# Performance work log

Measured on AMD Instinct MI355X. Metric: run time of the kernel, lower is better.

Reference implementation:

```python
import jax, jax.numpy as jnp
import numpy as np

D_MODEL = 2048
N_HEAD = 16
N_KV_HEAD = 4
D_HEAD = D_MODEL // N_HEAD          # 128
N_REP = N_HEAD // N_KV_HEAD        # 4
B, S = 2, 2048


def setup_inputs() -> dict:
    key = jax.random.key(0)
    ks = jax.random.split(key, 7)
    x = jax.random.normal(ks[0], (B, S, D_MODEL), dtype=jnp.float32)
    cos = jax.random.uniform(ks[1], (S, D_HEAD // 2), dtype=jnp.float32)
    sin = jax.random.uniform(ks[2], (S, D_HEAD // 2), dtype=jnp.float32)
    sc = 1.0 / np.sqrt(D_MODEL)
    # weights stored as [in, out] so projection is x @ W
    wq = jax.random.normal(ks[3], (D_MODEL, D_MODEL), dtype=jnp.float32) * sc
    wk = jax.random.normal(ks[4], (D_MODEL, N_KV_HEAD * D_HEAD), dtype=jnp.float32) * sc
    wv = jax.random.normal(ks[5], (D_MODEL, N_KV_HEAD * D_HEAD), dtype=jnp.float32) * sc
    wo = jax.random.normal(ks[6], (D_MODEL, D_MODEL), dtype=jnp.float32) * sc
    return {"x": x, "cos": cos, "sin": sin, "wq": wq, "wk": wk, "wv": wv, "wo": wo}


def _apply_rope(t, cos, sin):
    # t: [B, H, S, D_HEAD]; cos/sin: [S, D_HEAD//2]
    d = t.shape[-1] // 2
    t1, t2 = t[..., :d], t[..., d:]
    c = cos[None, None, :, :]
    s = sin[None, None, :, :]
    return jnp.concatenate([t1 * c - t2 * s, t2 * c + t1 * s], axis=-1)


def reference(x, cos, sin, wq, wk, wv, wo):
    b, s, _ = x.shape
    q = (x @ wq).reshape(b, s, N_HEAD, D_HEAD).transpose(0, 2, 1, 3)      # [B,H,S,d]
    k = (x @ wk).reshape(b, s, N_KV_HEAD, D_HEAD).transpose(0, 2, 1, 3)   # [B,Hk,S,d]
    v = (x @ wv).reshape(b, s, N_KV_HEAD, D_HEAD).transpose(0, 2, 1, 3)
    q = _apply_rope(q, cos, sin)
    k = _apply_rope(k, cos, sin)
    # group query heads by shared kv head (repeat_interleave => consecutive groups)
    qg = q.reshape(b, N_KV_HEAD, N_REP, s, D_HEAD)
    scale = 1.0 / jnp.sqrt(jnp.asarray(D_HEAD, dtype=q.dtype))
    scores = jnp.einsum('bkrsd,bktd->bkrst', qg, k) * scale               # [B,Hk,r,S,S]
    causal = jnp.tril(jnp.ones((s, s), dtype=bool))
    scores = jnp.where(causal, scores, jnp.asarray(-jnp.inf, dtype=scores.dtype))
    attn = jax.nn.softmax(scores, axis=-1)
    out = jnp.einsum('bkrst,bktd->bkrsd', attn, v)                        # [B,Hk,r,S,d]
    out = out.reshape(b, N_HEAD, s, D_HEAD).transpose(0, 2, 1, 3).reshape(b, s, D_MODEL)
    return out @ wo
```

## Files before the change

kernel.cpp:

```cpp
#include <hip/hip_runtime.h>
#include <stdint.h>

#define D_MODEL 2048
#define NHEAD 16
#define NKV 4
#define DHEAD 128
#define BB 2
#define SS 2048
#define MROWS (BB*SS)
#define NQKV 3072

typedef __bf16 bf16x8_t __attribute__((ext_vector_type(8)));
typedef float f32x4_t __attribute__((ext_vector_type(4)));
typedef float f32x16_t __attribute__((ext_vector_type(16)));
typedef unsigned short u16x8_t __attribute__((ext_vector_type(8)));
typedef unsigned short u16x4_t __attribute__((ext_vector_type(4)));
typedef unsigned int u32x4_t __attribute__((ext_vector_type(4)));

__device__ __forceinline__ unsigned short f2bf(float f) {
    return __builtin_bit_cast(unsigned short, (__bf16)f);
}
__device__ __forceinline__ float bf2f(unsigned short h) {
    union { uint32_t u; float f; } v; v.u = ((uint32_t)h) << 16;
    return v.f;
}
__device__ __forceinline__ unsigned int pack_bf2(float lo, float hi) {
    return (unsigned int)f2bf(lo) | ((unsigned int)f2bf(hi) << 16);
}

__device__ __forceinline__ void stage16(const unsigned short* g, unsigned short* l) {
    auto gp = (const __attribute__((address_space(1))) unsigned short*)(uintptr_t)g;
    auto lp = (__attribute__((address_space(3))) unsigned short*)(uint32_t)(uintptr_t)l;
    __builtin_amdgcn_global_load_lds(gp, lp, 16, 0, 0);
}
__device__ __forceinline__ bf16x8_t lds_frag(const unsigned short* p) {
    return __builtin_bit_cast(bf16x8_t, *(const u16x8_t*)p);
}

#define BAR()   do { __builtin_amdgcn_s_barrier(); asm volatile("" ::: "memory"); } while (0)
#define WAITL() asm volatile("s_waitcnt lgkmcnt(0)" ::: "memory")

__global__ void k_convert(const float* __restrict__ in, unsigned short* __restrict__ out, int n4) {
    int stride = gridDim.x * blockDim.x;
    for (int idx = blockIdx.x * blockDim.x + threadIdx.x; idx < n4; idx += stride) {
        float4 f = ((const float4*)in)[idx];
        u16x4_t o;
        o[0] = f2bf(f.x); o[1] = f2bf(f.y); o[2] = f2bf(f.z); o[3] = f2bf(f.w);
        ((u16x4_t*)out)[idx] = o;
    }
}

__global__ __launch_bounds__(256) void k_transpose(const float* __restrict__ in,
                                                   unsigned short* __restrict__ out,
                                                   int R, int C) {
    __shared__ unsigned short tile[64][72];
    const int c0 = blockIdx.x * 64, r0 = blockIdx.y * 64;
    const int t = threadIdx.x;
    #pragma unroll
    for (int i = 0; i < 4; i++) {
        int g = i * 256 + t;
        int r = g >> 4, c4 = (g & 15) * 4;
        float4 f = *(const float4*)&in[(size_t)(r0 + r) * C + c0 + c4];
        tile[r][c4 + 0] = f2bf(f.x); tile[r][c4 + 1] = f2bf(f.y);
        tile[r][c4 + 2] = f2bf(f.z); tile[r][c4 + 3] = f2bf(f.w);
    }
    __syncthreads();
    #pragma unroll
    for (int i = 0; i < 2; i++) {
        int g = i * 256 + t;
        int oc = g >> 3, r8 = (g & 7) * 8;
        u16x8_t o;
        #pragma unroll
        for (int k = 0; k < 8; k++) o[k] = tile[r8 + k][oc];
        *(u16x8_t*)&out[(size_t)(c0 + oc) * R + r0 + r8] = o;
    }
}

__global__ void k_rope(const unsigned short* __restrict__ in, const float* __restrict__ cosb,
                       const float* __restrict__ sinb, unsigned short* __restrict__ out,
                       int nheads, int in_row_stride, float scale) {
    int idx = blockIdx.x * blockDim.x + threadIdx.x;
    int total = BB * SS * nheads * 64;
    if (idx >= total) return;
    int d  = idx & 63;
    int hh = (idx >> 6) % nheads;
    int bs = (idx >> 6) / nheads;
    int s  = bs % SS, b = bs / SS;
    const unsigned short* ip = in + (size_t)(b * SS + s) * in_row_stride + hh * 128 + d;
    float t1 = bf2f(ip[0]), t2 = bf2f(ip[64]);
    float c = cosb[s * 64 + d], sn = sinb[s * 64 + d];
    unsigned short* op = out + ((size_t)(b * nheads + hh) * SS + s) * 128 + d;
    op[0]  = f2bf((t1 * c - t2 * sn) * scale);
    op[64] = f2bf((t2 * c + t1 * sn) * scale);
}

__global__ __launch_bounds__(256) void k_vtrans(const unsigned short* __restrict__ src,
                                                unsigned short* __restrict__ vt,
                                                int stride, int colbase) {
    const int s0 = blockIdx.x * 64;
    const int kvb = blockIdx.y;
    const int b = kvb >> 2, kv = kvb & 3;
    __shared__ unsigned short tile[64][136];
    const int t = threadIdx.x;
    #pragma unroll
    for (int i = 0; i < 4; i++) {
        int g = i * 256 + t;
        int sr = g >> 4, c8 = (g & 15) * 8;
        u16x8_t v = *(const u16x8_t*)&src[(size_t)(b * SS + s0 + sr) * stride + colbase + kv * 128 + c8];
        #pragma unroll
        for (int k = 0; k < 8; k++) tile[sr][c8 + k] = v[k];
    }
    __syncthreads();
    unsigned short* obase = vt + (size_t)kvb * DHEAD * SS;
    #pragma unroll
    for (int i = 0; i < 4; i++) {
        int g = i * 256 + t;
        int d = g >> 3, s8 = (g & 7) * 8;
        u16x8_t o;
        #pragma unroll
        for (int k = 0; k < 8; k++) o[k] = tile[s8 + k][d];
        *(u16x8_t*)&obase[(size_t)d * SS + s0 + s8] = o;
    }
}

template <bool OUTF32>
__global__ __launch_bounds__(512, 2) void k_gemm8(const unsigned short* __restrict__ A,
                                                  const unsigned short* __restrict__ Bt,
                                                  void* __restrict__ Cout,
                                                  int N, int K, int ntn) {
    __shared__ __align__(16) unsigned short As[2][256 * 64];
    __shared__ __align__(16) unsigned short Bs[2][256 * 64];
    const int nwg = gridDim.x, wg = blockIdx.x;
    const int qq = nwg >> 3, rr = nwg & 7;
    const int xcd = wg & 7, sid = wg >> 3;
    const int swg = (xcd < rr ? xcd * (qq + 1) : rr * (qq + 1) + (xcd - rr) * qq) + sid;
    const int m0 = (swg / ntn) * 256, n0 = (swg % ntn) * 256;

    const int tid = threadIdx.x, lane = tid & 63, wid = tid >> 6;
    const int lr = lane & 15, lg = lane >> 4;
    const int wr = (wid >> 2) * 128, wc = (wid & 3) * 64;
    const int NT = K >> 6;

    auto stage = [&](int tile, int pos) {
        int srcTile = tile < NT ? tile : NT - 1;
        bool isA = (pos == 0) || (pos == 3);
        int half = (pos >= 2) ? 1 : 0;
        const unsigned short* base = isA ? A : Bt;
        int row0 = (isA ? m0 : n0) + half * 128;
        unsigned short* lbase = (isA ? As[tile & 1] : Bs[tile & 1]) + half * 8192;
        int k0 = srcTile * 64;
        #pragma unroll
        for (int i = 0; i < 2; i++) {
            int g = i * 512 + tid;
            int row = g >> 3, p = g & 7;
            stage16(&base[(size_t)(row0 + row) * K + k0 + ((p ^ (row & 7)) * 8)],
                    &lbase[(i * 512 + wid * 64) * 8]);
        }
    };

    bf16x8_t aA[4][2], bLo[2][2], bHi[2][2];
    f32x4_t acc[8][4] = {};

    stage(0, 0); stage(0, 3); stage(0, 1); stage(0, 2);
    stage(1, 1); stage(1, 2);
    asm volatile("s_waitcnt vmcnt(4)" ::: "memory");
    BAR();

    for (int t = 0; t < NT; t++) {
        const unsigned short* as = As[t & 1];
        const unsigned short* bs = Bs[t & 1];
        #pragma unroll
        for (int i = 0; i < 4; i++)
          #pragma unroll
          for (int kk = 0; kk < 2; kk++) {
            int R = wr + i * 16 + lr;
            aA[i][kk] = lds_frag(&as[R * 64 + (((kk * 4 + lg) ^ (R & 7)) * 8)]);
          }
        #pragma unroll
        for (int j = 0; j < 2; j++)
          #pragma unroll
          for (int kk = 0; kk < 2; kk++) {
            int R = wc + j * 16 + lr;
            bLo[j][kk] = lds_frag(&bs[R * 64 + (((kk * 4 + lg) ^ (R & 7)) * 8)]);
          }
        stage(t + 1, 0);
        BAR(); WAITL();
        __builtin_amdgcn_s_setprio(1);
        #pragma unroll
        for (int kk = 0; kk < 2; kk++)
          #pragma unroll
          for (int i = 0; i < 4; i++)
            #pragma unroll
            for (int j = 0; j < 2; j++)
              acc[i][j] = __builtin_amdgcn_mfma_f32_16x16x32_bf16(aA[i][kk], bLo[j][kk], acc[i][j], 0, 0, 0);
        __builtin_amdgcn_s_setprio(0);
        BAR();
        #pragma unroll
        for (int j = 0; j < 2; j++)
          #pragma unroll
          for (int kk = 0; kk < 2; kk++) {
            int R = wc + (2 + j) * 16 + lr;
            bHi[j][kk] = lds_frag(&bs[R * 64 + (((kk * 4 + lg) ^ (R & 7)) * 8)]);
          }
        stage(t + 1, 3);
        BAR(); WAITL();
        __builtin_amdgcn_s_setprio(1);
        #pragma unroll
        for (int kk = 0; kk < 2; kk++)
          #pragma unroll
          for (int i = 0; i < 4; i++)
            #pragma unroll
            for (int j = 0; j < 2; j++)
              acc[i][2 + j] = __builtin_amdgcn_mfma_f32_16x16x32_bf16(aA[i][kk], bHi[j][kk], acc[i][2 + j], 0, 0, 0);
        __builtin_amdgcn_s_setprio(0);
        BAR();
        #pragma unroll
        for (int i = 0; i < 4; i++)
          #pragma unroll
          for (int kk = 0; kk < 2; kk++) {
            int R = wr + (4 + i) * 16 + lr;
            aA[i][kk] = lds_frag(&as[R * 64 + (((kk * 4 + lg) ^ (R & 7)) * 8)]);
          }
        stage(t + 2, 1);
        BAR(); WAITL();
        __builtin_amdgcn_s_setprio(1);
        #pragma unroll
        for (int kk = 0; kk < 2; kk++)
          #pragma unroll
          for (int i = 0; i < 4; i++)
            #pragma unroll
            for (int j = 0; j < 2; j++)
              acc[4 + i][2 + j] = __builtin_amdgcn_mfma_f32_16x16x32_bf16(aA[i][kk], bHi[j][kk], acc[4 + i][2 + j], 0, 0, 0);
        __builtin_amdgcn_s_setprio(0);
        BAR();
        stage(t + 2, 2);
        asm volatile("s_waitcnt vmcnt(4)" ::: "memory");
        BAR(); WAITL();
        __builtin_amdgcn_s_setprio(1);
        #pragma unroll
        for (int kk = 0; kk < 2; kk++)
          #pragma unroll
          for (int i = 0; i < 4; i++)
            #pragma unroll
            for (int j = 0; j < 2; j++)
              acc[4 + i][j] = __builtin_amdgcn_mfma_f32_16x16x32_bf16(aA[i][kk], bLo[j][kk], acc[4 + i][j], 0, 0, 0);
        __builtin_amdgcn_s_setprio(0);
        BAR();
    }

    #pragma unroll
    for (int m = 0; m < 8; m++)
      #pragma unroll
      for (int n = 0; n < 4; n++)
        #pragma unroll
        for (int r = 0; r < 4; r++) {
            int row = m0 + wr + m * 16 + lg * 4 + r;
            int col = n0 + wc + n * 16 + lr;
            if constexpr (OUTF32) ((float*)Cout)[(size_t)row * N + col] = acc[m][n][r];
            else ((unsigned short*)Cout)[(size_t)row * N + col] = f2bf(acc[m][n][r]);
        }
}

template <bool OUTF32>
__global__ __launch_bounds__(512, 2) void k_gemm8h(const unsigned short* __restrict__ A,
                                                   const unsigned short* __restrict__ Bt,
                                                   void* __restrict__ Cout,
                                                   int N, int K, int ntn) {
    __shared__ __align__(16) unsigned short As[2][128 * 64];
    __shared__ __align__(16) unsigned short Bs[2][256 * 64];
    const int nwg = gridDim.x, wg = blockIdx.x;
    const int qq = nwg >> 3, rr = nwg & 7;
    const int xcd = wg & 7, sid = wg >> 3;
    const int swg = (xcd < rr ? xcd * (qq + 1) : rr * (qq + 1) + (xcd - rr) * qq) + sid;
    const int m0 = (swg / ntn) * 128, n0 = (swg % ntn) * 256;

    const int tid = threadIdx.x, lane = tid & 63, wid = tid >> 6;
    const int lr = lane & 15, lg = lane >> 4;
    const int wr = (wid >> 2) * 64, wc = (wid & 3) * 64;
    const int NT = K >> 6;

    auto stage = [&](int tile, int pos) {
        int srcTile = tile < NT ? tile : NT - 1;
        bool isA = (pos == 0);
        const unsigned short* base = isA ? A : Bt;
        int row0 = isA ? m0 : (n0 + (pos - 1) * 128);
        unsigned short* lbase = isA ? As[tile & 1] : (Bs[tile & 1] + (pos - 1) * 8192);
        int k0 = srcTile * 64;
        #pragma unroll
        for (int i = 0; i < 2; i++) {
            int g = i * 512 + tid;
            int row = g >> 3, p = g & 7;
            stage16(&base[(size_t)(row0 + row) * K + k0 + ((p ^ (row & 7)) * 8)],
                    &lbase[(i * 512 + wid * 64) * 8]);
        }
    };

    bf16x8_t aA[2][2], bLo[2][2], bHi[2][2];
    f32x4_t acc[4][4] = {};

    stage(0, 0); stage(0, 1); stage(0, 2);
    stage(1, 1); stage(1, 2);
    asm volatile("s_waitcnt vmcnt(4)" ::: "memory");
    BAR();

    for (int t = 0; t < NT; t++) {
        const unsigned short* as = As[t & 1];
        const unsigned short* bs = Bs[t & 1];
        #pragma unroll
        for (int i = 0; i < 2; i++)
          #pragma unroll
          for (int kk = 0; kk < 2; kk++) {
            int R = wr + i * 16 + lr;
            aA[i][kk] = lds_frag(&as[R * 64 + (((kk * 4 + lg) ^ (R & 7)) * 8)]);
          }
        #pragma unroll
        for (int j = 0; j < 2; j++)
          #pragma unroll
          for (int kk = 0; kk < 2; kk++) {
            int R = wc + j * 16 + lr;
            bLo[j][kk] = lds_frag(&bs[R * 64 + (((kk * 4 + lg) ^ (R & 7)) * 8)]);
          }
        stage(t + 1, 0);
        BAR(); WAITL();
        __builtin_amdgcn_s_setprio(1);
        #pragma unroll
        for (int kk = 0; kk < 2; kk++)
          #pragma unroll
          for (int i = 0; i < 2; i++)
            #pragma unroll
            for (int j = 0; j < 2; j++)
              acc[i][j] = __builtin_amdgcn_mfma_f32_16x16x32_bf16(aA[i][kk], bLo[j][kk], acc[i][j], 0, 0, 0);
        __builtin_amdgcn_s_setprio(0);
        BAR();
        #pragma unroll
        for (int j = 0; j < 2; j++)
          #pragma unroll
          for (int kk = 0; kk < 2; kk++) {
            int R = wc + (2 + j) * 16 + lr;
            bHi[j][kk] = lds_frag(&bs[R * 64 + (((kk * 4 + lg) ^ (R & 7)) * 8)]);
          }
        BAR(); WAITL();
        __builtin_amdgcn_s_setprio(1);
        #pragma unroll
        for (int kk = 0; kk < 2; kk++)
          #pragma unroll
          for (int i = 0; i < 2; i++)
            #pragma unroll
            for (int j = 0; j < 2; j++)
              acc[i][2 + j] = __builtin_amdgcn_mfma_f32_16x16x32_bf16(aA[i][kk], bHi[j][kk], acc[i][2 + j], 0, 0, 0);
        __builtin_amdgcn_s_setprio(0);
        BAR();
        #pragma unroll
        for (int i = 0; i < 2; i++)
          #pragma unroll
          for (int kk = 0; kk < 2; kk++) {
            int R = wr + (2 + i) * 16 + lr;
            aA[i][kk] = lds_frag(&as[R * 64 + (((kk * 4 + lg) ^ (R & 7)) * 8)]);
          }
        stage(t + 2, 1);
        BAR(); WAITL();
        __builtin_amdgcn_s_setprio(1);
        #pragma unroll
        for (int kk = 0; kk < 2; kk++)
          #pragma unroll
          for (int i = 0; i < 2; i++)
            #pragma unroll
            for (int j = 0; j < 2; j++)
              acc[2 + i][2 + j] = __builtin_amdgcn_mfma_f32_16x16x32_bf16(aA[i][kk], bHi[j][kk], acc[2 + i][2 + j], 0, 0, 0);
        __builtin_amdgcn_s_setprio(0);
        BAR();
        stage(t + 2, 2);
        asm volatile("s_waitcnt vmcnt(4)" ::: "memory");
        BAR(); WAITL();
        __builtin_amdgcn_s_setprio(1);
        #pragma unroll
        for (int kk = 0; kk < 2; kk++)
          #pragma unroll
          for (int i = 0; i < 2; i++)
            #pragma unroll
            for (int j = 0; j < 2; j++)
              acc[2 + i][j] = __builtin_amdgcn_mfma_f32_16x16x32_bf16(aA[i][kk], bLo[j][kk], acc[2 + i][j], 0, 0, 0);
        __builtin_amdgcn_s_setprio(0);
        BAR();
    }

    #pragma unroll
    for (int m = 0; m < 4; m++)
      #pragma unroll
      for (int n = 0; n < 4; n++)
        #pragma unroll
        for (int r = 0; r < 4; r++) {
            int row = m0 + wr + m * 16 + lg * 4 + r;
            int col = n0 + wc + n * 16 + lr;
            if constexpr (OUTF32) ((float*)Cout)[(size_t)row * N + col] = acc[m][n][r];
            else ((unsigned short*)Cout)[(size_t)row * N + col] = f2bf(acc[m][n][r]);
        }
}

__global__ __launch_bounds__(256, 2) void k_attn(const unsigned short* __restrict__ qg,
                                                 const float* __restrict__ cosb,
                                                 const float* __restrict__ sinb,
                                                 const unsigned short* __restrict__ kb,
                                                 const unsigned short* __restrict__ vt,
                                                 unsigned short* __restrict__ ab) {
    const int bid = blockIdx.x;
    const int u = bid & 255;
    const int t = (bid < 256) ? (u >> 5) : (15 - (u >> 5));
    const int h = u & 15, b = (u >> 4) & 1;
    const int kvh = h >> 2;
    const int tid = threadIdx.x, lane = tid & 63, wid = tid >> 6;
    const int ql = lane & 31, hi = lane >> 5;
    const int swzq = ql & 7;
    __shared__ __align__(16) unsigned short k_lds[2][64 * 128];
    __shared__ __align__(16) unsigned short v_lds[2][128 * 64];
    __shared__ float sm_lds[128];

    const unsigned short* kbase = kb + (size_t)(b * NKV + kvh) * SS * DHEAD;
    const unsigned short* vbase = vt + (size_t)(b * NKV + kvh) * DHEAD * SS;

    auto stage_kv = [&](int j, int buf) {
        #pragma unroll
        for (int i = 0; i < 4; i++) {
            int g = i * 256 + wid * 64 + lane;
            int row = g >> 4, p = g & 15;
            stage16(&kbase[(size_t)(j * 64 + row) * DHEAD + ((p ^ (row & 7)) * 8)],
                    &k_lds[buf][(i * 256 + wid * 64) * 8]);
        }
        #pragma unroll
        for (int i = 0; i < 4; i++) {
            int g = i * 256 + wid * 64 + lane;
            int row = g >> 3, p = g & 7;
            stage16(&vbase[(size_t)row * SS + j * 64 + ((p ^ (row & 7)) * 8)],
                    &v_lds[buf][(i * 256 + wid * 64) * 8]);
        }
    };

    auto make_frag = [&](const f32x16_t& p, int base) -> bf16x8_t {
        unsigned int c01 = pack_bf2(p[base + 0], p[base + 1]);
        unsigned int c23 = pack_bf2(p[base + 2], p[base + 3]);
        unsigned int c45 = pack_bf2(p[base + 4], p[base + 5]);
        unsigned int c67 = pack_bf2(p[base + 6], p[base + 7]);
        unsigned int r1 = __shfl_xor(hi ? c01 : c45, 32);
        unsigned int r2 = __shfl_xor(hi ? c23 : c67, 32);
        u32x4_t w;
        w[0] = hi ? r1 : c01;
        w[1] = hi ? r2 : c23;
        w[2] = hi ? c45 : r1;
        w[3] = hi ? c67 : r2;
        return __builtin_bit_cast(bf16x8_t, w);
    };

    const int q0w = t * 128 + wid * 32;
    const int s_row = q0w + ql;
    const int jend = 2 * t + 1;

    bf16x8_t qf[8];
    {
        const unsigned short* qsrc = qg + (size_t)(b * SS + s_row) * NQKV + h * DHEAD;
        const float SCALE = 0.12751743f;
        #pragma unroll
        for (int kk = 0; kk < 4; kk++) {
            int dbase = kk * 16 + hi * 8;
            u16x8_t r1 = *(const u16x8_t*)&qsrc[dbase];
            u16x8_t r2 = *(const u16x8_t*)&qsrc[64 + dbase];
            float4 c0 = *(const float4*)&cosb[(size_t)s_row * 64 + dbase];
            float4 c1 = *(const float4*)&cosb[(size_t)s_row * 64 + dbase + 4];
            float4 s0 = *(const float4*)&sinb[(size_t)s_row * 64 + dbase];
            float4 s1 = *(const float4*)&sinb[(size_t)s_row * 64 + dbase + 4];
            float cc[8] = {c0.x, c0.y, c0.z, c0.w, c1.x, c1.y, c1.z, c1.w};
            float ss[8] = {s0.x, s0.y, s0.z, s0.w, s1.x, s1.y, s1.z, s1.w};
            #pragma unroll
            for (int e = 0; e < 8; e++) {
                float t1 = bf2f(r1[e]), t2 = bf2f(r2[e]);
                qf[kk][e]     = (__bf16)((t1 * cc[e] - t2 * ss[e]) * SCALE);
                qf[kk + 4][e] = (__bf16)((t2 * cc[e] + t1 * ss[e]) * SCALE);
            }
        }
    }

    f32x16_t acc[4] = {};
    float m_i = -1e30f, l_i = 0.f;

    stage_kv(0, 0);
    asm volatile("s_waitcnt vmcnt(0)" ::: "memory");
    __syncthreads();

    #pragma unroll 1
    for (int j = 0; j <= jend; j++) {
        const int buf = j & 1;
        if (j < jend) stage_kv(j + 1, buf ^ 1);
        if ((q0w + 31) >= (j << 6)) {
            const unsigned short* kl = k_lds[buf];
            const unsigned short* vl = v_lds[buf];
            f32x16_t p0 = {}, p1 = {};
            __builtin_amdgcn_s_setprio(1);
            #pragma unroll
            for (int kk = 0; kk < 8; kk++) {
                int c = ((2 * kk + hi) ^ swzq) * 8;
                bf16x8_t k0 = lds_frag(&kl[ql * 128 + c]);
                bf16x8_t k1 = lds_frag(&kl[(32 + ql) * 128 + c]);
                p0 = __builtin_amdgcn_mfma_f32_32x32x16_bf16(k0, qf[kk], p0, 0, 0, 0);
                p1 = __builtin_amdgcn_mfma_f32_32x32x16_bf16(k1, qf[kk], p1, 0, 0, 0);
            }
            __builtin_amdgcn_s_setprio(0);
            if ((j << 6) + 63 > q0w) {
                const int qg2 = q0w + ql;
                const int kvb = (j << 6) + 4 * hi;
                #pragma unroll
                for (int r = 0; r < 16; r++) {
                    int kvg = kvb + (r & 3) + 8 * (r >> 2);
                    if (kvg > qg2) p0[r] = -1e30f;
                    if (kvg + 32 > qg2) p1[r] = -1e30f;
                }
            }
            float mx = p0[0];
            #pragma unroll
            for (int r = 1; r < 16; r++) mx = fmaxf(mx, p0[r]);
            #pragma unroll
            for (int r = 0; r < 16; r++) mx = fmaxf(mx, p1[r]);
            mx = fmaxf(mx, __shfl_xor(mx, 32));
            if (__any(mx - m_i > 8.0f)) {
                float mnew = fmaxf(m_i, mx);
                float alpha = exp2f(m_i - mnew);
                l_i *= alpha; m_i = mnew;
                if (lane < 32) sm_lds[wid * 32 + lane] = alpha;
                WAITL();
                #pragma unroll
                for (int r = 0; r < 16; r++) {
                    float ar = sm_lds[wid * 32 + (r & 3) + 8 * (r >> 2) + 4 * hi];
                    #pragma unroll
                    for (int d = 0; d < 4; d++) acc[d][r] *= ar;
                }
            }
            float sum = 0.f;
            #pragma unroll
            for (int r = 0; r < 16; r++) { float v = exp2f(p0[r] - m_i); p0[r] = v; sum += v; }
            #pragma unroll
            for (int r = 0; r < 16; r++) { float v = exp2f(p1[r] - m_i); p1[r] = v; sum += v; }
            sum += __shfl_xor(sum, 32);
            l_i += sum;
            bf16x8_t pa[4];
            pa[0] = make_frag(p0, 0);
            pa[1] = make_frag(p0, 8);
            pa[2] = make_frag(p1, 0);
            pa[3] = make_frag(p1, 8);
            __builtin_amdgcn_s_setprio(1);
            #pragma unroll
            for (int ks = 0; ks < 4; ks++) {
                int cv = ((2 * ks + hi) ^ swzq) * 8;
                #pragma unroll
                for (int d = 0; d < 4; d++) {
                    bf16x8_t bv = lds_frag(&vl[(d * 32 + ql) * 64 + cv]);
                    acc[d] = __builtin_amdgcn_mfma_f32_32x32x16_bf16(pa[ks], bv, acc[d], 0, 0, 0);
                }
            }
            __builtin_amdgcn_s_setprio(0);
        }
        asm volatile("s_waitcnt vmcnt(0)" ::: "memory");
        __syncthreads();
    }

    if (lane < 32) sm_lds[wid * 32 + lane] = l_i;
    WAITL();
    #pragma unroll
    for (int r = 0; r < 16; r++) {
        float li = sm_lds[wid * 32 + (r & 3) + 8 * (r >> 2) + 4 * hi];
        float rl = 1.0f / li;
        int rowg = q0w + (r & 3) + 8 * (r >> 2) + 4 * hi;
        #pragma unroll
        for (int d = 0; d < 4; d++)
            ab[((size_t)b * SS + rowg) * D_MODEL + h * DHEAD + d * 32 + ql] =
                f2bf(acc[d][r] * rl);
    }
}

extern "C" void kernel_launch(void* const* d_in, const int* in_sizes, int n_in,
                              void* d_out, int out_size, void* d_ws, size_t ws_size,
                              hipStream_t stream) {
    const float* x    = (const float*)d_in[0];
    const float* cosb = (const float*)d_in[1];
    const float* sinb = (const float*)d_in[2];
    const float* wq   = (const float*)d_in[3];
    const float* wk   = (const float*)d_in[4];
    const float* wv   = (const float*)d_in[5];
    const float* wo   = (const float*)d_in[6];

    char* ws = (char*)d_ws;
    unsigned short* xb    = (unsigned short*)(ws + (size_t)0);
    unsigned short* wqkvT = (unsigned short*)(ws + ((size_t)16 << 20));
    unsigned short* woT   = (unsigned short*)(ws + ((size_t)28 << 20));
    unsigned short* qkvg  = (unsigned short*)(ws + ((size_t)36 << 20));
    unsigned short* abuf  = (unsigned short*)(ws + ((size_t)60 << 20));
    unsigned short* kbuf  = (unsigned short*)(ws + ((size_t)76 << 20));
    unsigned short* vtb   = (unsigned short*)(ws + ((size_t)80 << 20));

    k_convert<<<2048, 256, 0, stream>>>(x, xb, MROWS * D_MODEL / 4);
    k_transpose<<<dim3(32, 32), 256, 0, stream>>>(wq, wqkvT, D_MODEL, D_MODEL);
    k_transpose<<<dim3(8, 32), 256, 0, stream>>>(wk, wqkvT + (size_t)2048 * D_MODEL, D_MODEL, 512);
    k_transpose<<<dim3(8, 32), 256, 0, stream>>>(wv, wqkvT + (size_t)2560 * D_MODEL, D_MODEL, 512);
    k_transpose<<<dim3(32, 32), 256, 0, stream>>>(wo, woT, D_MODEL, D_MODEL);

    k_gemm8<false><<<16 * 12, 512, 0, stream>>>(xb, wqkvT, qkvg, NQKV, D_MODEL, 12);

    k_rope<<<(BB * SS * NKV * 64) / 256, 256, 0, stream>>>(qkvg + 2048, cosb, sinb, kbuf, NKV, NQKV, 1.0f);
    k_vtrans<<<dim3(32, 8), 256, 0, stream>>>(qkvg, vtb, NQKV, 2560);

    k_attn<<<512, 256, 0, stream>>>(qkvg, cosb, sinb, kbuf, vtb, abuf);

    k_gemm8h<true><<<32 * 8, 512, 0, stream>>>(abuf, woT, (float*)d_out, D_MODEL, D_MODEL, 8);
}
```

Measured before the change: 203.6 us.

## Merge weight transposes into one launch and remap attention blocks per XCD

Four separate weight-transpose launches become a single kernel that picks its source matrix from the block index, which saves launch overhead and gaps between kernels. The attention grid mapping is also reordered so that block ids sharing bid&7 (one XCD under round-robin dispatch) handle the same batch and KV head. This should keep each head's K/V tiles resident in that XCD's L2. Causal load balance is kept by pairing forward and reversed query tiles across the two halves of the grid.

```diff
diff --git a/kernel.cpp b/kernel.cpp
--- a/kernel.cpp
+++ b/kernel.cpp
@@ -50,11 +50,20 @@
     }
 }
 
-__global__ __launch_bounds__(256) void k_transpose(const float* __restrict__ in,
-                                                   unsigned short* __restrict__ out,
-                                                   int R, int C) {
+__global__ __launch_bounds__(256) void k_transpose_all(const float* __restrict__ wq,
+                                                       const float* __restrict__ wk,
+                                                       const float* __restrict__ wv,
+                                                       const float* __restrict__ wo,
+                                                       unsigned short* __restrict__ wqkvT,
+                                                       unsigned short* __restrict__ woT) {
+    int id = blockIdx.x;
+    const float* in; unsigned short* out; int R, C, cx, ry;
+    if (id < 1024)      { in = wq; out = wqkvT;                              R = 2048; C = 2048; cx = id & 31; ry = id >> 5; }
+    else if (id < 1280) { id -= 1024; in = wk; out = wqkvT + (size_t)2048 * 2048; R = 2048; C = 512; cx = id & 7; ry = id >> 3; }
+    else if (id < 1536) { id -= 1280; in = wv; out = wqkvT + (size_t)2560 * 2048; R = 2048; C = 512; cx = id & 7; ry = id >> 3; }
+    else                { id -= 1536; in = wo; out = woT;                    R = 2048; C = 2048; cx = id & 31; ry = id >> 5; }
+    const int c0 = cx * 64, r0 = ry * 64;
     __shared__ unsigned short tile[64][72];
-    const int c0 = blockIdx.x * 64, r0 = blockIdx.y * 64;
     const int t = threadIdx.x;
     #pragma unroll
     for (int i = 0; i < 4; i++) {
@@ -404,10 +413,12 @@
                                                  const unsigned short* __restrict__ vt,
                                                  unsigned short* __restrict__ ab) {
     const int bid = blockIdx.x;
-    const int u = bid & 255;
-    const int t = (bid < 256) ? (u >> 5) : (15 - (u >> 5));
-    const int h = u & 15, b = (u >> 4) & 1;
-    const int kvh = h >> 2;
+    const int xcd = bid & 7, sid = bid >> 3;
+    const int b = xcd >> 2, kvh = xcd & 3;
+    int t, hh;
+    if (sid < 32) { t = sid >> 1; hh = sid & 1; }
+    else { int s2 = sid - 32; t = 15 - (s2 >> 1); hh = 2 + (s2 & 1); }
+    const int h = kvh * 4 + hh;
     const int tid = threadIdx.x, lane = tid & 63, wid = tid >> 6;
     const int ql = lane & 31, hi = lane >> 5;
     const int swzq = ql & 7;
@@ -595,10 +606,7 @@
     unsigned short* vtb   = (unsigned short*)(ws + ((size_t)80 << 20));
 
     k_convert<<<2048, 256, 0, stream>>>(x, xb, MROWS * D_MODEL / 4);
-    k_transpose<<<dim3(32, 32), 256, 0, stream>>>(wq, wqkvT, D_MODEL, D_MODEL);
-    k_transpose<<<dim3(8, 32), 256, 0, stream>>>(wk, wqkvT + (size_t)2048 * D_MODEL, D_MODEL, 512);
-    k_transpose<<<dim3(8, 32), 256, 0, stream>>>(wv, wqkvT + (size_t)2560 * D_MODEL, D_MODEL, 512);
-    k_transpose<<<dim3(32, 32), 256, 0, stream>>>(wo, woT, D_MODEL, D_MODEL);
+    k_transpose_all<<<2560, 256, 0, stream>>>(wq, wk, wv, wo, wqkvT, woT);
 
     k_gemm8<false><<<16 * 12, 512, 0, stream>>>(xb, wqkvT, qkvg, NQKV, D_MODEL, 12);
 
```

New measurement: 196.5 us. 1.04x faster.
